# Performance work log

Measured on AMD Instinct MI355X. Metric: run time of the kernel, lower is better.

The kernel has to match this reference:

```python
import jax, jax.numpy as jnp
import numpy as np

N_NODES = 500_000
N_EDGES = 16_000_000
F_IN = 4
C = 4


def setup_inputs() -> dict:
    key = jax.random.key(0)
    ks = jax.random.split(key, 8)
    x = jax.random.normal(ks[0], (N_NODES, F_IN), dtype=jnp.float32)
    edge_index = jax.random.randint(ks[1], (2, N_EDGES), 0, N_NODES, dtype=jnp.int32)
    node = 1000  # node id whose incident edges are scored
    # GCNConv weights (PyG lin weight is [out,in]; math is x @ W with W=[in,out]) + separate bias
    W1 = jax.random.normal(ks[2], (F_IN, C), dtype=jnp.float32) * 0.5
    b1 = jnp.zeros((C,), dtype=jnp.float32)
    W2 = jax.random.normal(ks[3], (C, C), dtype=jnp.float32) * 0.5
    b2 = jnp.zeros((C,), dtype=jnp.float32)
    Wr = jax.random.normal(ks[4], (C, 1), dtype=jnp.float32) * 0.5
    br = jnp.zeros((1,), dtype=jnp.float32)
    return {"x": x, "edge_index": edge_index, "node": node,
            "W1": W1, "b1": b1, "W2": W2, "b2": b2, "Wr": Wr, "br": br}


def reference(x, edge_index, node, W1, b1, W2, b2, Wr, br):
    n = x.shape[0]
    src, dst = edge_index[0], edge_index[1]
    # GCN normalization with added self-loops (PyG gcn_norm, edge_weight=1)
    loop = jnp.arange(n, dtype=src.dtype)
    srcl = jnp.concatenate([src, loop])  # [E+N]
    dstl = jnp.concatenate([dst, loop])
    deg = jax.ops.segment_sum(jnp.ones(srcl.shape[0], dtype=x.dtype), dstl, num_segments=n)
    dinv = jnp.where(deg > 0, jax.lax.rsqrt(deg), jnp.zeros_like(deg))
    norm = (dinv[srcl] * dinv[dstl])[:, None]  # [E+N, 1]

    def gcn_conv(h, W, b):
        hW = h @ W                                  # tiny GEMM [N,C]
        msg = hW[srcl] * norm                       # edge gather + normalize [E+N, C]
        return jax.ops.segment_sum(msg, dstl, num_segments=n) + b  # scatter-add

    h = jax.nn.relu(gcn_conv(x, W1, b1))
    h = jax.nn.relu(gcn_conv(h, W2, b2))

    # Edges incident to `node`; softmax restricted to them (others masked out)
    mask = (src == node) | (dst == node)            # [E]
    targets = jnp.where(src == node, dst, src)      # other endpoint (node itself for self-loop)
    logits = (h[targets] @ Wr + br)[:, 0]           # [E]
    neg = jnp.finfo(logits.dtype).min
    score = jax.nn.softmax(jnp.where(mask, logits, neg))  # masked entries -> 0
    targets_out = jnp.where(mask, targets, -1)
    return score, targets_out
```

## Files before the change

kernel.cpp:

```cpp
#include <hip/hip_runtime.h>

#define CAP_I   65536
#define CAP_S1  (1 << 18)
#define CAP_L2  (1 << 20)
#define CAP_L1  (1 << 22)
#define LBUF    2560
#define FLUSH_THRESH 512
#define NWMAX   15680

typedef unsigned int uint;

__global__ void k_passA(const int4* __restrict__ src4, const int4* __restrict__ dst4, int nvec,
                        const int* __restrict__ nodep,
                        float4* __restrict__ out_score4, float4* __restrict__ out_tgt4,
                        int* __restrict__ cnts, int* __restrict__ le, int* __restrict__ lt) {
    int node = *nodep;
    int stride = gridDim.x * blockDim.x;
    const float4 zero = make_float4(0.f, 0.f, 0.f, 0.f);
    const float4 neg1 = make_float4(-1.f, -1.f, -1.f, -1.f);
    for (int v = blockIdx.x * blockDim.x + threadIdx.x; v < nvec; v += stride) {
        int4 s4 = src4[v];
        int4 d4 = dst4[v];
        out_score4[v] = zero;
        out_tgt4[v]   = neg1;
        int ss[4] = {s4.x, s4.y, s4.z, s4.w};
        int dd[4] = {d4.x, d4.y, d4.z, d4.w};
#pragma unroll
        for (int k = 0; k < 4; k++) {
            if (ss[k] == node || dd[k] == node) {
                int t = (ss[k] == node) ? dd[k] : ss[k];
                int pos = atomicAdd(&cnts[0], 1);
                if (pos < CAP_I) { le[pos] = v * 4 + k; lt[pos] = t; }
            }
        }
    }
}

__global__ void k_markT(const int* __restrict__ cnts, const int* __restrict__ lt,
                        uint* __restrict__ bmT, uint* __restrict__ bmS1,
                        uint* __restrict__ bmS0,
                        int* __restrict__ cnts_w, int* __restrict__ s1list) {
    int n = cnts[0]; if (n > CAP_I) n = CAP_I;
    for (int i = threadIdx.x; i < n; i += blockDim.x) {
        int t = lt[i];
        uint bit = 1u << (t & 31);
        atomicOr(&bmT[t >> 5], bit);
        uint old = atomicOr(&bmS1[t >> 5], bit);
        if (!(old & bit)) {
            atomicOr(&bmS0[t >> 5], bit);
            int p = atomicAdd(&cnts_w[2], 1);
            if (p < CAP_S1) s1list[p] = t;
        }
    }
}

__global__ __launch_bounds__(512) void k_passB(
        const int* __restrict__ src, const int4* __restrict__ dst4, int nvec, int NW,
        const uint* __restrict__ bmT, uint* __restrict__ bmS1, uint* __restrict__ bmS0,
        int* __restrict__ cnts, int* __restrict__ l2s, int* __restrict__ l2t,
        int* __restrict__ s1list) {
    __shared__ uint lT[NWMAX];
    __shared__ int bes[LBUF], bet[LBUF], bs1[LBUF];
    __shared__ int lcE, lcS, gbE, gbS;
    for (int i = threadIdx.x; i < NW; i += blockDim.x) lT[i] = bmT[i];
    if (threadIdx.x == 0) { lcE = 0; lcS = 0; }
    __syncthreads();
    int tid0 = blockIdx.x * blockDim.x + threadIdx.x;
    int stride = gridDim.x * blockDim.x;
    int itersU = (nvec + stride - 1) / stride;
    for (int it = 0; it < itersU; ++it) {
        int v = tid0 + it * stride;
        if (v < nvec) {
            int4 d4 = dst4[v];
            int dd[4] = {d4.x, d4.y, d4.z, d4.w};
#pragma unroll
            for (int k = 0; k < 4; k++) {
                int d = dd[k];
                if ((lT[d >> 5] >> (d & 31)) & 1u) {
                    int s = src[v * 4 + k];
                    int p = atomicAdd(&lcE, 1);
                    if (p < LBUF) { bes[p] = s; bet[p] = d; }
                    uint bit = 1u << (s & 31);
                    uint old = atomicOr(&bmS1[s >> 5], bit);
                    if (!(old & bit)) {
                        atomicOr(&bmS0[s >> 5], bit);
                        int q = atomicAdd(&lcS, 1);
                        if (q < LBUF) bs1[q] = s;
                    }
                }
            }
        }
        __syncthreads();
        if (lcE > FLUSH_THRESH || lcS > FLUSH_THRESH) {
            int nE = min(lcE, LBUF), nS = min(lcS, LBUF);
            if (threadIdx.x == 0) {
                gbE = atomicAdd(&cnts[1], nE);
                gbS = atomicAdd(&cnts[2], nS);
            }
            __syncthreads();
            for (int i = threadIdx.x; i < nE; i += blockDim.x) {
                int pos = gbE + i;
                if (pos < CAP_L2) { l2s[pos] = bes[i]; l2t[pos] = bet[i]; }
            }
            for (int i = threadIdx.x; i < nS; i += blockDim.x) {
                int pos = gbS + i;
                if (pos < CAP_S1) s1list[pos] = bs1[i];
            }
            __syncthreads();
            if (threadIdx.x == 0) { lcE = 0; lcS = 0; }
        }
        __syncthreads();
    }
    int nE = min(lcE, LBUF), nS = min(lcS, LBUF);
    if (nE > 0 || nS > 0) {
        if (threadIdx.x == 0) {
            gbE = atomicAdd(&cnts[1], nE);
            gbS = atomicAdd(&cnts[2], nS);
        }
        __syncthreads();
        for (int i = threadIdx.x; i < nE; i += blockDim.x) {
            int pos = gbE + i;
            if (pos < CAP_L2) { l2s[pos] = bes[i]; l2t[pos] = bet[i]; }
        }
        for (int i = threadIdx.x; i < nS; i += blockDim.x) {
            int pos = gbS + i;
            if (pos < CAP_S1) s1list[pos] = bs1[i];
        }
    }
}

__global__ __launch_bounds__(512) void k_passC(
        const int* __restrict__ src, const int4* __restrict__ dst4, int nvec, int NW,
        const uint* __restrict__ bmS1, uint* __restrict__ bmS0,
        int* __restrict__ cnts, int* __restrict__ l1s, int* __restrict__ l1t) {
    __shared__ uint lS1[NWMAX];
    __shared__ int lbs[LBUF], lbt[LBUF];
    __shared__ int lcnt, gbase;
    for (int i = threadIdx.x; i < NW; i += blockDim.x) lS1[i] = bmS1[i];
    if (threadIdx.x == 0) lcnt = 0;
    __syncthreads();
    int tid0 = blockIdx.x * blockDim.x + threadIdx.x;
    int stride = gridDim.x * blockDim.x;
    int itersU = (nvec + stride - 1) / stride;
    for (int it = 0; it < itersU; ++it) {
        int v = tid0 + it * stride;
        if (v < nvec) {
            int4 d4 = dst4[v];
            int dd[4] = {d4.x, d4.y, d4.z, d4.w};
#pragma unroll
            for (int k = 0; k < 4; k++) {
                int d = dd[k];
                if ((lS1[d >> 5] >> (d & 31)) & 1u) {
                    int s = src[v * 4 + k];
                    atomicOr(&bmS0[s >> 5], 1u << (s & 31));
                    int p = atomicAdd(&lcnt, 1);
                    if (p < LBUF) { lbs[p] = s; lbt[p] = d; }
                }
            }
        }
        __syncthreads();
        if (lcnt > FLUSH_THRESH) {
            int n = min(lcnt, LBUF);
            if (threadIdx.x == 0) gbase = atomicAdd(&cnts[3], n);
            __syncthreads();
            for (int i = threadIdx.x; i < n; i += blockDim.x) {
                int pos = gbase + i;
                if (pos < CAP_L1) { l1s[pos] = lbs[i]; l1t[pos] = lbt[i]; }
            }
            __syncthreads();
            if (threadIdx.x == 0) lcnt = 0;
        }
        __syncthreads();
    }
    int n = min(lcnt, LBUF);
    if (n > 0) {
        if (threadIdx.x == 0) gbase = atomicAdd(&cnts[3], n);
        __syncthreads();
        for (int i = threadIdx.x; i < n; i += blockDim.x) {
            int pos = gbase + i;
            if (pos < CAP_L1) { l1s[pos] = lbs[i]; l1t[pos] = lbt[i]; }
        }
    }
}

__global__ __launch_bounds__(512) void k_passD(
        const int4* __restrict__ dst4, int nvec, int NW,
        const uint* __restrict__ bmS0, int* __restrict__ deg) {
    __shared__ uint lS0[NWMAX];
    for (int i = threadIdx.x; i < NW; i += blockDim.x) lS0[i] = bmS0[i];
    __syncthreads();
    int stride = gridDim.x * blockDim.x;
    for (int v = blockIdx.x * blockDim.x + threadIdx.x; v < nvec; v += stride) {
        int4 d4 = dst4[v];
        int dd[4] = {d4.x, d4.y, d4.z, d4.w};
#pragma unroll
        for (int k = 0; k < 4; k++) {
            int d = dd[k];
            if ((lS0[d >> 5] >> (d & 31)) & 1u) atomicAdd(&deg[d], 1);
        }
    }
}

__global__ void k_conv1(const int* __restrict__ cnts, const int* __restrict__ l1s,
                        const int* __restrict__ l1t, const float* __restrict__ x,
                        const float* __restrict__ W1, const int* __restrict__ deg,
                        float* __restrict__ acc1) {
    int n = cnts[3]; if (n > CAP_L1) n = CAP_L1;
    int stride = gridDim.x * blockDim.x;
    for (int j = blockIdx.x * blockDim.x + threadIdx.x; j < n; j += stride) {
        int s = l1s[j], d = l1t[j];
        float4 xv = *(const float4*)(x + (size_t)s * 4);
        float dis = rsqrtf((float)deg[s] + 1.0f);
        float o0 = (xv.x * W1[0] + xv.y * W1[4] + xv.z * W1[8]  + xv.w * W1[12]) * dis;
        float o1 = (xv.x * W1[1] + xv.y * W1[5] + xv.z * W1[9]  + xv.w * W1[13]) * dis;
        float o2 = (xv.x * W1[2] + xv.y * W1[6] + xv.z * W1[10] + xv.w * W1[14]) * dis;
        float o3 = (xv.x * W1[3] + xv.y * W1[7] + xv.z * W1[11] + xv.w * W1[15]) * dis;
        float* a = acc1 + (size_t)d * 4;
        atomicAdd(a + 0, o0); atomicAdd(a + 1, o1);
        atomicAdd(a + 2, o2); atomicAdd(a + 3, o3);
    }
}

__global__ void k_h1(const int* __restrict__ cnts, const int* __restrict__ s1list,
                     const float* __restrict__ x, const float* __restrict__ W1,
                     const float* __restrict__ b1, const float* __restrict__ W2,
                     const int* __restrict__ deg, const float* __restrict__ acc1,
                     float* __restrict__ gB) {
    int n = cnts[2]; if (n > CAP_S1) n = CAP_S1;
    int stride = gridDim.x * blockDim.x;
    for (int j = blockIdx.x * blockDim.x + threadIdx.x; j < n; j += stride) {
        int i = s1list[j];
        float di = rsqrtf((float)deg[i] + 1.0f);
        float4 xv = *(const float4*)(x + (size_t)i * 4);
        float4 a  = *(const float4*)(acc1 + (size_t)i * 4);
        float w0 = xv.x * W1[0] + xv.y * W1[4] + xv.z * W1[8]  + xv.w * W1[12];
        float w1 = xv.x * W1[1] + xv.y * W1[5] + xv.z * W1[9]  + xv.w * W1[13];
        float w2 = xv.x * W1[2] + xv.y * W1[6] + xv.z * W1[10] + xv.w * W1[14];
        float w3 = xv.x * W1[3] + xv.y * W1[7] + xv.z * W1[11] + xv.w * W1[15];
        float h0 = fmaxf((a.x + w0 * di) * di + b1[0], 0.f);
        float h1 = fmaxf((a.y + w1 * di) * di + b1[1], 0.f);
        float h2 = fmaxf((a.z + w2 * di) * di + b1[2], 0.f);
        float h3 = fmaxf((a.w + w3 * di) * di + b1[3], 0.f);
        float4 o;
        o.x = (h0 * W2[0] + h1 * W2[4] + h2 * W2[8]  + h3 * W2[12]) * di;
        o.y = (h0 * W2[1] + h1 * W2[5] + h2 * W2[9]  + h3 * W2[13]) * di;
        o.z = (h0 * W2[2] + h1 * W2[6] + h2 * W2[10] + h3 * W2[14]) * di;
        o.w = (h0 * W2[3] + h1 * W2[7] + h2 * W2[11] + h3 * W2[15]) * di;
        *(float4*)(gB + (size_t)i * 4) = o;
    }
}

__global__ void k_conv2(const int* __restrict__ cnts, const int* __restrict__ l2s,
                        const int* __restrict__ l2t, const float* __restrict__ gB,
                        float* __restrict__ acc2) {
    int n = cnts[1]; if (n > CAP_L2) n = CAP_L2;
    int stride = gridDim.x * blockDim.x;
    for (int j = blockIdx.x * blockDim.x + threadIdx.x; j < n; j += stride) {
        int s = l2s[j], t = l2t[j];
        float4 g = *(const float4*)(gB + (size_t)s * 4);
        float* a = acc2 + (size_t)t * 4;
        atomicAdd(a + 0, g.x); atomicAdd(a + 1, g.y);
        atomicAdd(a + 2, g.z); atomicAdd(a + 3, g.w);
    }
}

__global__ void k_z(const int* __restrict__ cnts, const int* __restrict__ lt,
                    const float* __restrict__ b2, const float* __restrict__ Wr,
                    const float* __restrict__ br, const int* __restrict__ deg,
                    const float* __restrict__ acc2, const float* __restrict__ gB,
                    float* __restrict__ z) {
    int n = cnts[0]; if (n > CAP_I) n = CAP_I;
    int stride = gridDim.x * blockDim.x;
    for (int j = blockIdx.x * blockDim.x + threadIdx.x; j < n; j += stride) {
        int t = lt[j];
        float di = rsqrtf((float)deg[t] + 1.0f);
        float4 a = *(const float4*)(acc2 + (size_t)t * 4);
        float4 g = *(const float4*)(gB + (size_t)t * 4);
        float h0 = fmaxf((a.x + g.x) * di + b2[0], 0.f);
        float h1 = fmaxf((a.y + g.y) * di + b2[1], 0.f);
        float h2 = fmaxf((a.z + g.z) * di + b2[2], 0.f);
        float h3 = fmaxf((a.w + g.w) * di + b2[3], 0.f);
        z[t] = h0 * Wr[0] + h1 * Wr[1] + h2 * Wr[2] + h3 * Wr[3] + br[0];
    }
}

__global__ void k_softmax(const int* __restrict__ cnts, const int* __restrict__ le,
                          const int* __restrict__ lt, const float* __restrict__ z,
                          float* __restrict__ out_score, float* __restrict__ out_tgt) {
    if (blockIdx.x != 0 || threadIdx.x != 0) return;
    int n = cnts[0]; if (n > CAP_I) n = CAP_I;
    float m = -3.402823466e+38f;
    for (int k = 0; k < n; k++) m = fmaxf(m, z[lt[k]]);
    float ssum = 0.f;
    for (int k = 0; k < n; k++) ssum += __expf(z[lt[k]] - m);
    float inv = (ssum > 0.f) ? 1.f / ssum : 0.f;
    for (int k = 0; k < n; k++) {
        out_score[le[k]] = __expf(z[lt[k]] - m) * inv;
        out_tgt[le[k]]   = (float)lt[k];
    }
}

extern "C" void kernel_launch(void* const* d_in, const int* in_sizes, int n_in,
                              void* d_out, int out_size, void* d_ws, size_t ws_size,
                              hipStream_t stream) {
    const float* x  = (const float*)d_in[0];
    const int*   ei = (const int*)d_in[1];
    const int*   nodep = (const int*)d_in[2];
    const float* W1 = (const float*)d_in[3];
    const float* b1 = (const float*)d_in[4];
    const float* W2 = (const float*)d_in[5];
    const float* b2 = (const float*)d_in[6];
    const float* Wr = (const float*)d_in[7];
    const float* br = (const float*)d_in[8];

    const int N = in_sizes[0] / 4;
    const int E = in_sizes[1] / 2;
    const int nvec = E / 4;
    const int NW = (N + 31) / 32;
    const int* src = ei;
    const int* dst = ei + E;

    char* ws = (char*)d_ws;
    size_t off = 0;
    auto alloc = [&](size_t bytes) { char* p = ws + off; off = (off + bytes + 255) & ~(size_t)255; return p; };
    char* zero_base = ws;
    int*   deg    = (int*)  alloc((size_t)N * 4);
    float* acc1   = (float*)alloc((size_t)N * 16);
    float* acc2   = (float*)alloc((size_t)N * 16);
    uint*  bmT    = (uint*) alloc((size_t)NW * 4);
    uint*  bmS1   = (uint*) alloc((size_t)NW * 4);
    uint*  bmS0   = (uint*) alloc((size_t)NW * 4);
    int*   cnts   = (int*)  alloc(256);
    size_t zero_len = off;
    float* gB     = (float*)alloc((size_t)N * 16);
    float* z      = (float*)alloc((size_t)N * 4);
    int*   le     = (int*)  alloc((size_t)CAP_I * 4);
    int*   lt     = (int*)  alloc((size_t)CAP_I * 4);
    int*   s1list = (int*)  alloc((size_t)CAP_S1 * 4);
    int*   l2s    = (int*)  alloc((size_t)CAP_L2 * 4);
    int*   l2t    = (int*)  alloc((size_t)CAP_L2 * 4);
    int*   l1s    = (int*)  alloc((size_t)CAP_L1 * 4);
    int*   l1t    = (int*)  alloc((size_t)CAP_L1 * 4);

    float* out_score = (float*)d_out;
    float* out_tgt   = out_score + E;

    int edgeBlocksA = (nvec + 255) / 256;
    if (edgeBlocksA > 2048) edgeBlocksA = 2048;
    const int listBlocks = 256;

    hipMemsetAsync(zero_base, 0, zero_len, stream);

    k_passA<<<edgeBlocksA, 256, 0, stream>>>((const int4*)src, (const int4*)dst, nvec, nodep,
                                             (float4*)out_score, (float4*)out_tgt, cnts, le, lt);
    k_markT<<<1, 256, 0, stream>>>(cnts, lt, bmT, bmS1, bmS0, cnts, s1list);
    k_passB<<<512, 512, 0, stream>>>(src, (const int4*)dst, nvec, NW, bmT, bmS1, bmS0,
                                     cnts, l2s, l2t, s1list);
    k_passC<<<512, 512, 0, stream>>>(src, (const int4*)dst, nvec, NW, bmS1, bmS0,
                                     cnts, l1s, l1t);
    k_passD<<<1024, 512, 0, stream>>>((const int4*)dst, nvec, NW, bmS0, deg);
    k_conv1<<<listBlocks, 256, 0, stream>>>(cnts, l1s, l1t, x, W1, deg, acc1);
    k_h1<<<listBlocks, 256, 0, stream>>>(cnts, s1list, x, W1, b1, W2, deg, acc1, gB);
    k_conv2<<<listBlocks, 256, 0, stream>>>(cnts, l2s, l2t, gB, acc2);
    k_z<<<listBlocks, 256, 0, stream>>>(cnts, lt, b2, Wr, br, deg, acc2, gB, z);
    k_softmax<<<1, 64, 0, stream>>>(cnts, le, lt, z, out_score, out_tgt);
}
```

Before: 303.4 us.

## Sparse-zero accumulators, move output init to passD, fuse tail kernels into one block

Drops the full-size memset of deg/acc1/acc2 and instead zeroes only the entries of newly discovered frontier nodes inside markT, passB and passC. Moves the output initialisation from passA into passD using nontemporal stores, and reads the bitmap from global memory instead of staging it in LDS. Fuses h1, conv2, z and softmax into a single one-block kernel to cut launch overhead. The single 1024-thread block serialises the tail work, which could be slow if the frontier lists are large.

```diff
diff --git a/kernel.cpp b/kernel.cpp
--- a/kernel.cpp
+++ b/kernel.cpp
@@ -9,20 +9,16 @@
 #define NWMAX   15680
 
 typedef unsigned int uint;
+typedef float vfloat4 __attribute__((ext_vector_type(4)));
 
 __global__ void k_passA(const int4* __restrict__ src4, const int4* __restrict__ dst4, int nvec,
                         const int* __restrict__ nodep,
-                        float4* __restrict__ out_score4, float4* __restrict__ out_tgt4,
                         int* __restrict__ cnts, int* __restrict__ le, int* __restrict__ lt) {
     int node = *nodep;
     int stride = gridDim.x * blockDim.x;
-    const float4 zero = make_float4(0.f, 0.f, 0.f, 0.f);
-    const float4 neg1 = make_float4(-1.f, -1.f, -1.f, -1.f);
     for (int v = blockIdx.x * blockDim.x + threadIdx.x; v < nvec; v += stride) {
         int4 s4 = src4[v];
         int4 d4 = dst4[v];
-        out_score4[v] = zero;
-        out_tgt4[v]   = neg1;
         int ss[4] = {s4.x, s4.y, s4.z, s4.w};
         int dd[4] = {d4.x, d4.y, d4.z, d4.w};
 #pragma unroll
@@ -39,8 +35,11 @@
 __global__ void k_markT(const int* __restrict__ cnts, const int* __restrict__ lt,
                         uint* __restrict__ bmT, uint* __restrict__ bmS1,
                         uint* __restrict__ bmS0,
-                        int* __restrict__ cnts_w, int* __restrict__ s1list) {
+                        int* __restrict__ cnts_w, int* __restrict__ s1list,
+                        int* __restrict__ deg, float4* __restrict__ acc1,
+                        float4* __restrict__ acc2) {
     int n = cnts[0]; if (n > CAP_I) n = CAP_I;
+    const float4 z4 = make_float4(0.f, 0.f, 0.f, 0.f);
     for (int i = threadIdx.x; i < n; i += blockDim.x) {
         int t = lt[i];
         uint bit = 1u << (t & 31);
@@ -48,6 +47,7 @@
         uint old = atomicOr(&bmS1[t >> 5], bit);
         if (!(old & bit)) {
             atomicOr(&bmS0[t >> 5], bit);
+            deg[t] = 0; acc1[t] = z4; acc2[t] = z4;
             int p = atomicAdd(&cnts_w[2], 1);
             if (p < CAP_S1) s1list[p] = t;
         }
@@ -58,13 +58,15 @@
         const int* __restrict__ src, const int4* __restrict__ dst4, int nvec, int NW,
         const uint* __restrict__ bmT, uint* __restrict__ bmS1, uint* __restrict__ bmS0,
         int* __restrict__ cnts, int* __restrict__ l2s, int* __restrict__ l2t,
-        int* __restrict__ s1list) {
+        int* __restrict__ s1list,
+        int* __restrict__ deg, float4* __restrict__ acc1, float4* __restrict__ acc2) {
     __shared__ uint lT[NWMAX];
     __shared__ int bes[LBUF], bet[LBUF], bs1[LBUF];
     __shared__ int lcE, lcS, gbE, gbS;
     for (int i = threadIdx.x; i < NW; i += blockDim.x) lT[i] = bmT[i];
     if (threadIdx.x == 0) { lcE = 0; lcS = 0; }
     __syncthreads();
+    const float4 z4 = make_float4(0.f, 0.f, 0.f, 0.f);
     int tid0 = blockIdx.x * blockDim.x + threadIdx.x;
     int stride = gridDim.x * blockDim.x;
     int itersU = (nvec + stride - 1) / stride;
@@ -84,6 +86,7 @@
                     uint old = atomicOr(&bmS1[s >> 5], bit);
                     if (!(old & bit)) {
                         atomicOr(&bmS0[s >> 5], bit);
+                        deg[s] = 0; acc1[s] = z4; acc2[s] = z4;
                         int q = atomicAdd(&lcS, 1);
                         if (q < LBUF) bs1[q] = s;
                     }
@@ -132,7 +135,8 @@
 __global__ __launch_bounds__(512) void k_passC(
         const int* __restrict__ src, const int4* __restrict__ dst4, int nvec, int NW,
         const uint* __restrict__ bmS1, uint* __restrict__ bmS0,
-        int* __restrict__ cnts, int* __restrict__ l1s, int* __restrict__ l1t) {
+        int* __restrict__ cnts, int* __restrict__ l1s, int* __restrict__ l1t,
+        int* __restrict__ deg) {
     __shared__ uint lS1[NWMAX];
     __shared__ int lbs[LBUF], lbt[LBUF];
     __shared__ int lcnt, gbase;
@@ -152,7 +156,9 @@
                 int d = dd[k];
                 if ((lS1[d >> 5] >> (d & 31)) & 1u) {
                     int s = src[v * 4 + k];
-                    atomicOr(&bmS0[s >> 5], 1u << (s & 31));
+                    uint bit = 1u << (s & 31);
+                    uint old = atomicOr(&bmS0[s >> 5], bit);
+                    if (!(old & bit)) deg[s] = 0;
                     int p = atomicAdd(&lcnt, 1);
                     if (p < LBUF) { lbs[p] = s; lbt[p] = d; }
                 }
@@ -183,20 +189,22 @@
     }
 }
 
-__global__ __launch_bounds__(512) void k_passD(
-        const int4* __restrict__ dst4, int nvec, int NW,
-        const uint* __restrict__ bmS0, int* __restrict__ deg) {
-    __shared__ uint lS0[NWMAX];
-    for (int i = threadIdx.x; i < NW; i += blockDim.x) lS0[i] = bmS0[i];
-    __syncthreads();
+__global__ __launch_bounds__(256) void k_passD(
+        const int4* __restrict__ dst4, int nvec,
+        const uint* __restrict__ bmS0, int* __restrict__ deg,
+        vfloat4* __restrict__ out_score4, vfloat4* __restrict__ out_tgt4) {
+    const vfloat4 zero = {0.f, 0.f, 0.f, 0.f};
+    const vfloat4 neg1 = {-1.f, -1.f, -1.f, -1.f};
     int stride = gridDim.x * blockDim.x;
     for (int v = blockIdx.x * blockDim.x + threadIdx.x; v < nvec; v += stride) {
         int4 d4 = dst4[v];
+        __builtin_nontemporal_store(zero, &out_score4[v]);
+        __builtin_nontemporal_store(neg1, &out_tgt4[v]);
         int dd[4] = {d4.x, d4.y, d4.z, d4.w};
 #pragma unroll
         for (int k = 0; k < 4; k++) {
             int d = dd[k];
-            if ((lS0[d >> 5] >> (d & 31)) & 1u) atomicAdd(&deg[d], 1);
+            if ((bmS0[d >> 5] >> (d & 31)) & 1u) atomicAdd(&deg[d], 1);
         }
     }
 }
@@ -221,14 +229,20 @@
     }
 }
 
-__global__ void k_h1(const int* __restrict__ cnts, const int* __restrict__ s1list,
-                     const float* __restrict__ x, const float* __restrict__ W1,
-                     const float* __restrict__ b1, const float* __restrict__ W2,
-                     const int* __restrict__ deg, const float* __restrict__ acc1,
-                     float* __restrict__ gB) {
-    int n = cnts[2]; if (n > CAP_S1) n = CAP_S1;
-    int stride = gridDim.x * blockDim.x;
-    for (int j = blockIdx.x * blockDim.x + threadIdx.x; j < n; j += stride) {
+__global__ __launch_bounds__(1024) void k_tail(
+        const int* __restrict__ cnts, const int* __restrict__ s1list,
+        const int* __restrict__ l2s, const int* __restrict__ l2t,
+        const int* __restrict__ le, const int* __restrict__ lt,
+        const float* __restrict__ x, const float* __restrict__ W1,
+        const float* __restrict__ b1, const float* __restrict__ W2,
+        const float* __restrict__ b2, const float* __restrict__ Wr,
+        const float* __restrict__ br, const int* __restrict__ deg,
+        const float* __restrict__ acc1, float* __restrict__ acc2,
+        float* __restrict__ gB, float* __restrict__ z,
+        float* __restrict__ out_score, float* __restrict__ out_tgt) {
+    int tid = threadIdx.x;
+    int n2 = cnts[2]; if (n2 > CAP_S1) n2 = CAP_S1;
+    for (int j = tid; j < n2; j += blockDim.x) {
         int i = s1list[j];
         float di = rsqrtf((float)deg[i] + 1.0f);
         float4 xv = *(const float4*)(x + (size_t)i * 4);
@@ -248,30 +262,18 @@
         o.w = (h0 * W2[3] + h1 * W2[7] + h2 * W2[11] + h3 * W2[15]) * di;
         *(float4*)(gB + (size_t)i * 4) = o;
     }
-}
-
-__global__ void k_conv2(const int* __restrict__ cnts, const int* __restrict__ l2s,
-                        const int* __restrict__ l2t, const float* __restrict__ gB,
-                        float* __restrict__ acc2) {
-    int n = cnts[1]; if (n > CAP_L2) n = CAP_L2;
-    int stride = gridDim.x * blockDim.x;
-    for (int j = blockIdx.x * blockDim.x + threadIdx.x; j < n; j += stride) {
+    __syncthreads();
+    int nL2 = cnts[1]; if (nL2 > CAP_L2) nL2 = CAP_L2;
+    for (int j = tid; j < nL2; j += blockDim.x) {
         int s = l2s[j], t = l2t[j];
         float4 g = *(const float4*)(gB + (size_t)s * 4);
         float* a = acc2 + (size_t)t * 4;
         atomicAdd(a + 0, g.x); atomicAdd(a + 1, g.y);
         atomicAdd(a + 2, g.z); atomicAdd(a + 3, g.w);
     }
-}
-
-__global__ void k_z(const int* __restrict__ cnts, const int* __restrict__ lt,
-                    const float* __restrict__ b2, const float* __restrict__ Wr,
-                    const float* __restrict__ br, const int* __restrict__ deg,
-                    const float* __restrict__ acc2, const float* __restrict__ gB,
-                    float* __restrict__ z) {
-    int n = cnts[0]; if (n > CAP_I) n = CAP_I;
-    int stride = gridDim.x * blockDim.x;
-    for (int j = blockIdx.x * blockDim.x + threadIdx.x; j < n; j += stride) {
+    __syncthreads();
+    int nI = cnts[0]; if (nI > CAP_I) nI = CAP_I;
+    for (int j = tid; j < nI; j += blockDim.x) {
         int t = lt[j];
         float di = rsqrtf((float)deg[t] + 1.0f);
         float4 a = *(const float4*)(acc2 + (size_t)t * 4);
@@ -282,21 +284,17 @@
         float h3 = fmaxf((a.w + g.w) * di + b2[3], 0.f);
         z[t] = h0 * Wr[0] + h1 * Wr[1] + h2 * Wr[2] + h3 * Wr[3] + br[0];
     }
-}
-
-__global__ void k_softmax(const int* __restrict__ cnts, const int* __restrict__ le,
-                          const int* __restrict__ lt, const float* __restrict__ z,
-                          float* __restrict__ out_score, float* __restrict__ out_tgt) {
-    if (blockIdx.x != 0 || threadIdx.x != 0) return;
-    int n = cnts[0]; if (n > CAP_I) n = CAP_I;
-    float m = -3.402823466e+38f;
-    for (int k = 0; k < n; k++) m = fmaxf(m, z[lt[k]]);
-    float ssum = 0.f;
-    for (int k = 0; k < n; k++) ssum += __expf(z[lt[k]] - m);
-    float inv = (ssum > 0.f) ? 1.f / ssum : 0.f;
-    for (int k = 0; k < n; k++) {
-        out_score[le[k]] = __expf(z[lt[k]] - m) * inv;
-        out_tgt[le[k]]   = (float)lt[k];
+    __syncthreads();
+    if (tid == 0) {
+        float m = -3.402823466e+38f;
+        for (int k = 0; k < nI; k++) m = fmaxf(m, z[lt[k]]);
+        float ssum = 0.f;
+        for (int k = 0; k < nI; k++) ssum += __expf(z[lt[k]] - m);
+        float inv = (ssum > 0.f) ? 1.f / ssum : 0.f;
+        for (int k = 0; k < nI; k++) {
+            out_score[le[k]] = __expf(z[lt[k]] - m) * inv;
+            out_tgt[le[k]]   = (float)lt[k];
+        }
     }
 }
 
@@ -324,14 +322,14 @@
     size_t off = 0;
     auto alloc = [&](size_t bytes) { char* p = ws + off; off = (off + bytes + 255) & ~(size_t)255; return p; };
     char* zero_base = ws;
-    int*   deg    = (int*)  alloc((size_t)N * 4);
-    float* acc1   = (float*)alloc((size_t)N * 16);
-    float* acc2   = (float*)alloc((size_t)N * 16);
     uint*  bmT    = (uint*) alloc((size_t)NW * 4);
     uint*  bmS1   = (uint*) alloc((size_t)NW * 4);
     uint*  bmS0   = (uint*) alloc((size_t)NW * 4);
     int*   cnts   = (int*)  alloc(256);
     size_t zero_len = off;
+    int*   deg    = (int*)  alloc((size_t)N * 4);
+    float* acc1   = (float*)alloc((size_t)N * 16);
+    float* acc2   = (float*)alloc((size_t)N * 16);
     float* gB     = (float*)alloc((size_t)N * 16);
     float* z      = (float*)alloc((size_t)N * 4);
     int*   le     = (int*)  alloc((size_t)CAP_I * 4);
@@ -349,19 +347,20 @@
     if (edgeBlocksA > 2048) edgeBlocksA = 2048;
     const int listBlocks = 256;
 
-    hipMemsetAsync(zero_base, 0, zero_len, stream);
+    (void)hipMemsetAsync(zero_base, 0, zero_len, stream);
 
     k_passA<<<edgeBlocksA, 256, 0, stream>>>((const int4*)src, (const int4*)dst, nvec, nodep,
-                                             (float4*)out_score, (float4*)out_tgt, cnts, le, lt);
-    k_markT<<<1, 256, 0, stream>>>(cnts, lt, bmT, bmS1, bmS0, cnts, s1list);
+                                             cnts, le, lt);
+    k_markT<<<1, 256, 0, stream>>>(cnts, lt, bmT, bmS1, bmS0, cnts, s1list,
+                                   deg, (float4*)acc1, (float4*)acc2);
     k_passB<<<512, 512, 0, stream>>>(src, (const int4*)dst, nvec, NW, bmT, bmS1, bmS0,
-                                     cnts, l2s, l2t, s1list);
+                                     cnts, l2s, l2t, s1list,
+                                     deg, (float4*)acc1, (float4*)acc2);
     k_passC<<<512, 512, 0, stream>>>(src, (const int4*)dst, nvec, NW, bmS1, bmS0,
-                                     cnts, l1s, l1t);
-    k_passD<<<1024, 512, 0, stream>>>((const int4*)dst, nvec, NW, bmS0, deg);
+                                     cnts, l1s, l1t, deg);
+    k_passD<<<2048, 256, 0, stream>>>((const int4*)dst, nvec, bmS0, deg,
+                                      (vfloat4*)out_score, (vfloat4*)out_tgt);
     k_conv1<<<listBlocks, 256, 0, stream>>>(cnts, l1s, l1t, x, W1, deg, acc1);
-    k_h1<<<listBlocks, 256, 0, stream>>>(cnts, s1list, x, W1, b1, W2, deg, acc1, gB);
-    k_conv2<<<listBlocks, 256, 0, stream>>>(cnts, l2s, l2t, gB, acc2);
-    k_z<<<listBlocks, 256, 0, stream>>>(cnts, lt, b2, Wr, br, deg, acc2, gB, z);
-    k_softmax<<<1, 64, 0, stream>>>(cnts, le, lt, z, out_score, out_tgt);
-}
+    k_tail<<<1, 1024, 0, stream>>>(cnts, s1list, l2s, l2t, le, lt, x, W1, b1, W2, b2,
+                                   Wr, br, deg, acc1, acc2, gB, z, out_score, out_tgt);
+}
```

After: 329.5 us. 1.09x slower.
